# Kernel optimization log

Hardware: AMD Instinct MI355X
Metric: run time of the kernel (lower is better)

## Reference

```python
import jax, jax.numpy as jnp
import numpy as np


def setup_inputs() -> dict:
    key = jax.random.key(0)
    ks = jax.random.split(key, 6)
    B, F, E, H, U = 64, 4096, 256, 512, 512
    scale = 0.02
    return {
        "features": jax.random.normal(ks[0], (B, F, E), dtype=jnp.float32),
        "hidden": jax.random.normal(ks[1], (B, H), dtype=jnp.float32),
        "W1_w": jax.random.normal(ks[2], (E, U), dtype=jnp.float32) * scale,
        "W1_b": jnp.zeros((U,), dtype=jnp.float32),
        "W2_w": jax.random.normal(ks[3], (H, U), dtype=jnp.float32) * scale,
        "W2_b": jnp.zeros((U,), dtype=jnp.float32),
        "V_w": jax.random.normal(ks[4], (U, 1), dtype=jnp.float32) * scale,
        "V_b": jnp.zeros((1,), dtype=jnp.float32),
    }


def reference(features, hidden, W1_w, W1_b, W2_w, W2_b, V_w, V_b):
    # features: (B, F, E); hidden: (B, H)
    proj_f = jnp.einsum("bfe,eu->bfu", features, W1_w) + W1_b          # (B, F, U)
    proj_h = (hidden @ W2_w + W2_b)[:, None, :]                        # (B, 1, U)
    attention_hidden = jnp.tanh(proj_f + proj_h)                       # (B, F, U)
    scores = jnp.einsum("bfu,uo->bfo", attention_hidden, V_w) + V_b    # (B, F, 1)
    attention_weights = jax.nn.softmax(scores, axis=1)                 # (B, F, 1)
    context_vector = jnp.sum(attention_weights * features, axis=1)     # (B, E)
    return (context_vector, attention_weights)
```

## Files before the change

kernel.cpp:

```cpp
#include <hip/hip_runtime.h>
#include <cmath>

constexpr int Bdim = 64;
constexpr int Fdim = 4096;
constexpr int Edim = 256;
constexpr int Hdim = 512;
constexpr int Udim = 512;

typedef __attribute__((ext_vector_type(8))) short short8;
typedef __attribute__((ext_vector_type(4))) float f32x4;

__device__ __forceinline__ unsigned short f2bf(float f) {
    unsigned int u = __float_as_uint(f);
    u += 0x7FFFu + ((u >> 16) & 1u);
    return (unsigned short)(u >> 16);
}
__device__ __forceinline__ unsigned int pack2(float lo, float hi) {
    return (unsigned int)f2bf(lo) | ((unsigned int)f2bf(hi) << 16);
}
__device__ __forceinline__ float tanh_fast(float x) {
    float e = __expf(2.0f * x);
    return 1.0f - 2.0f * __builtin_amdgcn_rcpf(e + 1.0f);
}
__device__ __forceinline__ void gload_lds16(const void* g, void* l) {
    __builtin_amdgcn_global_load_lds(
        (const __attribute__((address_space(1))) unsigned int*)g,
        (__attribute__((address_space(3))) unsigned int*)l, 16, 0, 0);
}

__global__ __launch_bounds__(256) void prep_kernel(
    const float* __restrict__ hidden, const float* __restrict__ W2,
    const float* __restrict__ W1b, const float* __restrict__ W2b,
    float* __restrict__ cb,
    const float* __restrict__ W1, unsigned short* __restrict__ Th,
    float* __restrict__ ctx, const int do_t)
{
    const int bid = blockIdx.x;
    const int tid = threadIdx.x;

    if (bid < 128) {
        const int b = bid >> 1;
        const int u = (bid & 1) * 256 + tid;
        const float* hb = hidden + (size_t)b * Hdim;
        float acc = 0.f;
        #pragma unroll 8
        for (int h = 0; h < Hdim; ++h)
            acc = fmaf(hb[h], W2[(size_t)h * Udim + u], acc);
        cb[(size_t)b * Udim + u] = acc + W1b[u] + W2b[u];
    } else if (bid < 160) {
        if (!do_t) return;
        __shared__ unsigned short sT[64][72];
        const int k  = bid - 128;
        const int e0 = (k & 3) * 64, u0 = (k >> 2) * 64;
        const int ue = tid & 63, er = tid >> 6;
        #pragma unroll
        for (int it = 0; it < 16; ++it) {
            const int e = er + it * 4;
            sT[ue][e] = f2bf(W1[(size_t)(e0 + e) * Udim + u0 + ue]);
        }
        __syncthreads();
        const int ur = tid >> 2, cq = tid & 3;
        const int u = u0 + ur, s = u & 7;
        const int cA = (e0 >> 3) + cq * 2;
        uint4 a  = *(const uint4*)&sT[ur][cq * 16];
        uint4 b2 = *(const uint4*)&sT[ur][cq * 16 + 8];
        unsigned short* dst = Th + (size_t)u * Edim;
        *(uint4*)(dst + ((cA ^ s) << 3))       = a;
        *(uint4*)(dst + (((cA + 1) ^ s) << 3)) = b2;
    } else {
        const int idx = (bid - 160) * 256 + tid;
        ((float4*)ctx)[idx] = make_float4(0.f, 0.f, 0.f, 0.f);
    }
}

__global__ __launch_bounds__(256, 4) void score_mfma4_kernel(
    const float* __restrict__ feat,
    const unsigned short* __restrict__ W1Ts,
    const float* __restrict__ Vw, const float* __restrict__ Vb,
    const float* __restrict__ cb, float* __restrict__ scr,
    float* __restrict__ pm, float* __restrict__ ps, float* __restrict__ pc)
{
    __shared__ unsigned short lds[16896];

    const int b    = blockIdx.y;
    const int fc   = blockIdx.x;
    const int f0   = fc * 64;
    const int tid  = threadIdx.x;
    const int lane = tid & 63;
    const int w    = tid >> 6;
    const int ln15 = lane & 15;
    const int kq   = lane >> 4;
    const int swz  = ln15 & 7;

    short8 af[8];
    {
        unsigned short* sAw = lds + w * 4224;
        const float* gA = feat + ((size_t)(b * Fdim + f0 + w * 16)) * Edim;
        #pragma unroll
        for (int r = 0; r < 16; ++r) {
            float4 v = *(const float4*)(gA + (size_t)r * Edim + lane * 4);
            uint2 p; p.x = pack2(v.x, v.y); p.y = pack2(v.z, v.w);
            *(uint2*)&sAw[r * 264 + lane * 4] = p;
        }
        #pragma unroll
        for (int k8 = 0; k8 < 8; ++k8)
            af[k8] = *(const short8*)&sAw[ln15 * 264 + k8 * 32 + kq * 8];
    }
    __syncthreads();

    float sacc[4] = {};
    const float* cbB = cb + (size_t)b * Udim;

    {
        const char* gB = (const char*)W1Ts;
        #pragma unroll
        for (int t = 0; t < 4; ++t) {
            const int chunk = w * 4 + t;
            gload_lds16(gB + (size_t)chunk * 1024 + lane * 16,
                        (char*)lds + chunk * 1024);
        }
    }
    __syncthreads();

    for (int p = 0; p < 16; ++p) {
        if (p < 15) {
            const char* gB = (const char*)(W1Ts + (size_t)(p + 1) * 32 * Edim);
            char* lb = (char*)lds + ((p + 1) & 1) * 16384;
            #pragma unroll
            for (int t = 0; t < 4; ++t) {
                const int chunk = w * 4 + t;
                gload_lds16(gB + (size_t)chunk * 1024 + lane * 16,
                            lb + chunk * 1024);
            }
        }

        const unsigned short* bw = lds + (p & 1) * 8192;
        const int ub = p * 32;
        const float cu0 = cbB[ub + ln15],     cu1 = cbB[ub + 16 + ln15];
        const float vv0 = Vw[ub + ln15],      vv1 = Vw[ub + 16 + ln15];
        f32x4 acc0 = {}, acc1 = {};
        #pragma unroll
        for (int k8 = 0; k8 < 8; ++k8) {
            const int co = ((k8 * 4 + kq) ^ swz) * 8;
            short8 b0 = *(const short8*)&bw[ln15 * 256 + co];
            short8 b1 = *(const short8*)&bw[(16 + ln15) * 256 + co];
            acc0 = __builtin_amdgcn_mfma_f32_16x16x32_bf16(af[k8], b0, acc0, 0, 0, 0);
            acc1 = __builtin_amdgcn_mfma_f32_16x16x32_bf16(af[k8], b1, acc1, 0, 0, 0);
        }
        #pragma unroll
        for (int r = 0; r < 4; ++r)
            sacc[r] += tanh_fast(acc0[r] + cu0) * vv0
                     + tanh_fast(acc1[r] + cu1) * vv1;

        if (p < 15) __syncthreads();
    }

    float* sF = (float*)lds;
    float* wl = (float*)lds + 64;
    float4* sred = (float4*)((char*)lds + 1024);

    const float vb = Vb[0];
    #pragma unroll
    for (int r = 0; r < 4; ++r) {
        float s = sacc[r];
        s += __shfl_xor(s, 1);
        s += __shfl_xor(s, 2);
        s += __shfl_xor(s, 4);
        s += __shfl_xor(s, 8);
        if (ln15 == 0) {
            const int fr = w * 16 + kq * 4 + r;
            const float sv = s + vb;
            scr[(size_t)b * Fdim + f0 + fr] = sv;
            sF[fr] = sv;
        }
    }
    __syncthreads();

    if (tid < 64) {
        const float sc = sF[tid];
        float m = sc;
        #pragma unroll
        for (int off = 1; off < 64; off <<= 1)
            m = fmaxf(m, __shfl_xor(m, off));
        const float wv = expf(sc - m);
        float sm = wv;
        #pragma unroll
        for (int off = 1; off < 64; off <<= 1)
            sm += __shfl_xor(sm, off);
        wl[tid] = wv;
        if (tid == 0) {
            pm[b * 64 + fc] = m;
            ps[b * 64 + fc] = sm;
        }
    }
    __syncthreads();

    const int e4 = tid & 63;
    const int fg = tid >> 6;
    const float4* fp = (const float4*)(feat + ((size_t)b * Fdim + f0) * Edim);

    float4 a = make_float4(0.f, 0.f, 0.f, 0.f);
    #pragma unroll
    for (int i = 0; i < 16; ++i) {
        const int f = i * 4 + fg;
        const float4 fv = fp[(size_t)f * 64 + e4];
        const float wv = wl[f];
        a.x = fmaf(wv, fv.x, a.x);
        a.y = fmaf(wv, fv.y, a.y);
        a.z = fmaf(wv, fv.z, a.z);
        a.w = fmaf(wv, fv.w, a.w);
    }
    sred[tid] = a;
    __syncthreads();

    if (fg == 0) {
        const float4 r0 = sred[e4];
        const float4 r1 = sred[64 + e4];
        const float4 r2 = sred[128 + e4];
        const float4 r3 = sred[192 + e4];
        float4 o;
        o.x = r0.x + r1.x + r2.x + r3.x;
        o.y = r0.y + r1.y + r2.y + r3.y;
        o.z = r0.z + r1.z + r2.z + r3.z;
        o.w = r0.w + r1.w + r2.w + r3.w;
        *(float4*)&pc[((size_t)b * 64 + fc) * 256 + e4 * 4] = o;
    }
}

__global__ __launch_bounds__(256) void merge_kernel(
    const float* __restrict__ scr, const float* __restrict__ pm,
    const float* __restrict__ ps, const float* __restrict__ pc,
    float* __restrict__ wts, float* __restrict__ ctx)
{
    __shared__ float sscale[64];
    __shared__ float sms[2];

    const int b   = blockIdx.x;
    const int tid = threadIdx.x;

    if (tid < 64) {
        const float mi = pm[b * 64 + tid];
        float m = mi;
        #pragma unroll
        for (int off = 1; off < 64; off <<= 1)
            m = fmaxf(m, __shfl_xor(m, off));
        const float sc = expf(mi - m);
        float s = ps[b * 64 + tid] * sc;
        #pragma unroll
        for (int off = 1; off < 64; off <<= 1)
            s += __shfl_xor(s, off);
        sscale[tid] = sc;
        if (tid == 0) { sms[0] = m; sms[1] = 1.0f / s; }
    }
    __syncthreads();
    const float m   = sms[0];
    const float inv = sms[1];

    {
        float c = 0.f;
        const float* p = pc + (size_t)b * 64 * 256 + tid;
        #pragma unroll 8
        for (int i = 0; i < 64; ++i)
            c = fmaf(p[(size_t)i * 256], sscale[i], c);
        ctx[(size_t)b * Edim + tid] = c * inv;
    }

    const float* row  = scr + (size_t)b * Fdim;
    float*       wrow = wts + (size_t)b * Fdim;
    #pragma unroll
    for (int i = 0; i < 16; ++i) {
        const float v = row[tid + 256 * i];
        wrow[tid + 256 * i] = expf(v - m) * inv;
    }
}

constexpr int TFt = 64;
constexpr int TUt = 64;
constexpr int LDR = Edim + 4;

__global__ __launch_bounds__(256) void score_kernel(
    const float* __restrict__ feat, const float* __restrict__ W1,
    const float* __restrict__ Vw, const float* __restrict__ Vb,
    const float* __restrict__ cb, float* __restrict__ scores)
{
    __shared__ float sA[TFt * LDR];
    __shared__ float sW[TUt * LDR];

    const int b   = blockIdx.y;
    const int f0  = blockIdx.x * TFt;
    const int tid = threadIdx.x;
    const int tf  = tid >> 4;
    const int tu  = tid & 15;

    {
        const float4* gA = (const float4*)(feat + ((size_t)b * Fdim + f0) * Edim);
        #pragma unroll
        for (int it = 0; it < 16; ++it) {
            const int i = tid + it * 256;
            const int f = i >> 6;
            const int qq = i & 63;
            const float4 v = gA[i];
            *(float4*)&sA[f * LDR + 4 * qq] = v;
        }
    }

    float sacc[4] = {0.f, 0.f, 0.f, 0.f};
    const float* cbb = cb + (size_t)b * Udim;

    for (int uc = 0; uc < Udim; uc += TUt) {
        __syncthreads();
        #pragma unroll
        for (int it = 0; it < 16; ++it) {
            const int i = tid + it * 256;
            const int e = i >> 4;
            const int qq = i & 15;
            const float4 v = *(const float4*)(W1 + (size_t)e * Udim + uc + 4 * qq);
            sW[(4 * qq + 0) * LDR + e] = v.x;
            sW[(4 * qq + 1) * LDR + e] = v.y;
            sW[(4 * qq + 2) * LDR + e] = v.z;
            sW[(4 * qq + 3) * LDR + e] = v.w;
        }
        __syncthreads();

        float acc[4][4] = {};
        #pragma unroll 4
        for (int e = 0; e < Edim; e += 4) {
            float4 a0 = *(const float4*)&sA[(tf +  0) * LDR + e];
            float4 a1 = *(const float4*)&sA[(tf + 16) * LDR + e];
            float4 a2 = *(const float4*)&sA[(tf + 32) * LDR + e];
            float4 a3 = *(const float4*)&sA[(tf + 48) * LDR + e];
            float4 w0 = *(const float4*)&sW[(tu +  0) * LDR + e];
            float4 w1 = *(const float4*)&sW[(tu + 16) * LDR + e];
            float4 w2 = *(const float4*)&sW[(tu + 32) * LDR + e];
            float4 w3 = *(const float4*)&sW[(tu + 48) * LDR + e];
            #define FMA4(i, j, A, W)                         \
                acc[i][j] = fmaf(A.x, W.x, acc[i][j]);       \
                acc[i][j] = fmaf(A.y, W.y, acc[i][j]);       \
                acc[i][j] = fmaf(A.z, W.z, acc[i][j]);       \
                acc[i][j] = fmaf(A.w, W.w, acc[i][j]);
            FMA4(0,0,a0,w0) FMA4(0,1,a0,w1) FMA4(0,2,a0,w2) FMA4(0,3,a0,w3)
            FMA4(1,0,a1,w0) FMA4(1,1,a1,w1) FMA4(1,2,a1,w2) FMA4(1,3,a1,w3)
            FMA4(2,0,a2,w0) FMA4(2,1,a2,w1) FMA4(2,2,a2,w2) FMA4(2,3,a2,w3)
            FMA4(3,0,a3,w0) FMA4(3,1,a3,w1) FMA4(3,2,a3,w2) FMA4(3,3,a3,w3)
            #undef FMA4
        }

        #pragma unroll
        for (int j = 0; j < 4; ++j) {
            const int u = uc + tu + 16 * j;
            const float vw = Vw[u];
            const float cuv = cbb[u];
            #pragma unroll
            for (int i = 0; i < 4; ++i)
                sacc[i] = fmaf(tanhf(acc[i][j] + cuv), vw, sacc[i]);
        }
    }

    const float vb = Vb[0];
    #pragma unroll
    for (int i = 0; i < 4; ++i) {
        float s = sacc[i];
        s += __shfl_xor(s, 1);
        s += __shfl_xor(s, 2);
        s += __shfl_xor(s, 4);
        s += __shfl_xor(s, 8);
        if (tu == 0)
            scores[(size_t)b * Fdim + f0 + tf + 16 * i] = s + vb;
    }
}

__global__ __launch_bounds__(256) void softmax_kernel(float* __restrict__ sc)
{
    __shared__ float red[256];
    const int b = blockIdx.x;
    const int tid = threadIdx.x;
    float* row = sc + (size_t)b * Fdim;

    float v[16];
    float m = -INFINITY;
    #pragma unroll
    for (int i = 0; i < 16; ++i) {
        v[i] = row[tid + 256 * i];
        m = fmaxf(m, v[i]);
    }
    red[tid] = m;
    __syncthreads();
    for (int s = 128; s > 0; s >>= 1) {
        if (tid < s) red[tid] = fmaxf(red[tid], red[tid + s]);
        __syncthreads();
    }
    m = red[0];
    __syncthreads();

    float sum = 0.f;
    #pragma unroll
    for (int i = 0; i < 16; ++i) {
        v[i] = expf(v[i] - m);
        sum += v[i];
    }
    red[tid] = sum;
    __syncthreads();
    for (int s = 128; s > 0; s >>= 1) {
        if (tid < s) red[tid] += red[tid + s];
        __syncthreads();
    }
    const float inv = 1.f / red[0];
    #pragma unroll
    for (int i = 0; i < 16; ++i)
        row[tid + 256 * i] = v[i] * inv;
}

__global__ __launch_bounds__(256) void context_kernel(
    const float* __restrict__ feat, const float* __restrict__ wts,
    float* __restrict__ ctx)
{
    const int b  = blockIdx.y;
    const int fc = blockIdx.x;
    const int e  = threadIdx.x;

    const float* fp = feat + ((size_t)b * Fdim + (size_t)fc * 256) * Edim + e;
    const float* wp = wts + (size_t)b * Fdim + (size_t)fc * 256;

    float acc = 0.f;
    #pragma unroll 8
    for (int f = 0; f < 256; ++f)
        acc = fmaf(wp[f], fp[(size_t)f * Edim], acc);

    atomicAdd(&ctx[(size_t)b * Edim + e], acc);
}

extern "C" void kernel_launch(void* const* d_in, const int* in_sizes, int n_in,
                              void* d_out, int out_size, void* d_ws, size_t ws_size,
                              hipStream_t stream)
{
    const float* features = (const float*)d_in[0];
    const float* hidden   = (const float*)d_in[1];
    const float* W1w      = (const float*)d_in[2];
    const float* W1b      = (const float*)d_in[3];
    const float* W2w      = (const float*)d_in[4];
    const float* W2b      = (const float*)d_in[5];
    const float* Vw       = (const float*)d_in[6];
    const float* Vb       = (const float*)d_in[7];

    float* ctx = (float*)d_out;
    float* wts = (float*)d_out + (size_t)Bdim * Edim;

    float*          cb   = (float*)d_ws;
    unsigned short* W1Ts = (unsigned short*)((char*)d_ws + 131072);
    float*          scr  = (float*)((char*)d_ws + 393216);
    float*          pm   = (float*)((char*)d_ws + 1441792);
    float*          ps   = (float*)((char*)d_ws + 1458176);
    float*          pc   = (float*)((char*)d_ws + 1474560);
    const size_t NEED = 1474560 + (size_t)Bdim * 64 * Edim * sizeof(float);
    const int mfma_ok = (ws_size >= NEED) ? 1 : 0;

    prep_kernel<<<176, 256, 0, stream>>>(hidden, W2w, W1b, W2b, cb,
                                         W1w, W1Ts, ctx, mfma_ok);

    if (mfma_ok) {
        dim3 sgrid(Fdim / 64, Bdim);
        score_mfma4_kernel<<<sgrid, 256, 0, stream>>>(features, W1Ts, Vw, Vb, cb,
                                                      scr, pm, ps, pc);
        merge_kernel<<<Bdim, 256, 0, stream>>>(scr, pm, ps, pc, wts, ctx);
    } else {
        dim3 sgrid(Fdim / TFt, Bdim);
        score_kernel<<<sgrid, 256, 0, stream>>>(features, W1w, Vw, Vb, cb, wts);
        softmax_kernel<<<Bdim, 256, 0, stream>>>(wts);
        dim3 cgrid(16, Bdim);
        context_kernel<<<cgrid, 256, 0, stream>>>(features, wts, ctx);
    }
}
```

Measured before the change: 464.6 us.

## Use 2-wave blocks with 32 rows per wave sharing each W1 fragment

```diff
diff --git a/kernel.cpp b/kernel.cpp
--- a/kernel.cpp
+++ b/kernel.cpp
@@ -1,4 +1,5 @@
 #include <hip/hip_runtime.h>
+#include <hip/hip_bf16.h>
 #include <cmath>
 
 constexpr int Bdim = 64;
@@ -16,7 +17,8 @@
     return (unsigned short)(u >> 16);
 }
 __device__ __forceinline__ unsigned int pack2(float lo, float hi) {
-    return (unsigned int)f2bf(lo) | ((unsigned int)f2bf(hi) << 16);
+    __hip_bfloat162 h2 = __float22bfloat162_rn(make_float2(lo, hi));
+    return *reinterpret_cast<unsigned int*>(&h2);
 }
 __device__ __forceinline__ float tanh_fast(float x) {
     float e = __expf(2.0f * x);
@@ -73,14 +75,14 @@
     }
 }
 
-__global__ __launch_bounds__(256, 4) void score_mfma4_kernel(
+__global__ __launch_bounds__(128, 4) void score_mfma4_kernel(
     const float* __restrict__ feat,
     const unsigned short* __restrict__ W1Ts,
     const float* __restrict__ Vw, const float* __restrict__ Vb,
     const float* __restrict__ cb, float* __restrict__ scr,
     float* __restrict__ pm, float* __restrict__ ps, float* __restrict__ pc)
 {
-    __shared__ unsigned short lds[16896];
+    __shared__ unsigned short lds[8192];
 
     const int b    = blockIdx.y;
     const int fc   = blockIdx.x;
@@ -92,97 +94,97 @@
     const int kq   = lane >> 4;
     const int swz  = ln15 & 7;
 
-    short8 af[8];
+    #pragma unroll
+    for (int t = 0; t < 4; ++t)
+        gload_lds16((const char*)W1Ts + (size_t)(tid + t * 128) * 16,
+                    (char*)lds + (tid + t * 128) * 16);
+
+    short8 af[2][8];
     {
-        unsigned short* sAw = lds + w * 4224;
-        const float* gA = feat + ((size_t)(b * Fdim + f0 + w * 16)) * Edim;
-        #pragma unroll
-        for (int r = 0; r < 16; ++r) {
-            float4 v = *(const float4*)(gA + (size_t)r * Edim + lane * 4);
-            uint2 p; p.x = pack2(v.x, v.y); p.y = pack2(v.z, v.w);
-            *(uint2*)&sAw[r * 264 + lane * 4] = p;
-        }
-        #pragma unroll
-        for (int k8 = 0; k8 < 8; ++k8)
-            af[k8] = *(const short8*)&sAw[ln15 * 264 + k8 * 32 + kq * 8];
-    }
-    __syncthreads();
-
-    float sacc[4] = {};
+        const float* gA = feat +
+            ((size_t)(b * Fdim + f0 + w * 32 + ln15)) * Edim + kq * 8;
+        #pragma unroll
+        for (int h = 0; h < 2; ++h) {
+            #pragma unroll 4
+            for (int k8 = 0; k8 < 8; ++k8) {
+                const float* p = gA + (size_t)h * 16 * Edim + k8 * 32;
+                const float4 v0 = *(const float4*)(p);
+                const float4 v1 = *(const float4*)(p + 4);
+                uint4 uu;
+                uu.x = pack2(v0.x, v0.y);
+                uu.y = pack2(v0.z, v0.w);
+                uu.z = pack2(v1.x, v1.y);
+                uu.w = pack2(v1.z, v1.w);
+                af[h][k8] = *reinterpret_cast<short8*>(&uu);
+            }
+        }
+    }
+    __syncthreads();
+
+    float sacc[2][4] = {};
     const float* cbB = cb + (size_t)b * Udim;
 
-    {
-        const char* gB = (const char*)W1Ts;
-        #pragma unroll
-        for (int t = 0; t < 4; ++t) {
-            const int chunk = w * 4 + t;
-            gload_lds16(gB + (size_t)chunk * 1024 + lane * 16,
-                        (char*)lds + chunk * 1024);
-        }
-    }
-    __syncthreads();
-
-    for (int p = 0; p < 16; ++p) {
-        if (p < 15) {
-            const char* gB = (const char*)(W1Ts + (size_t)(p + 1) * 32 * Edim);
-            char* lb = (char*)lds + ((p + 1) & 1) * 16384;
+    for (int p = 0; p < 32; ++p) {
+        if (p < 31) {
+            const char* gB = (const char*)(W1Ts + (size_t)(p + 1) * 16 * Edim);
+            char* lb = (char*)lds + ((p + 1) & 1) * 8192;
             #pragma unroll
-            for (int t = 0; t < 4; ++t) {
-                const int chunk = w * 4 + t;
-                gload_lds16(gB + (size_t)chunk * 1024 + lane * 16,
-                            lb + chunk * 1024);
-            }
-        }
-
-        const unsigned short* bw = lds + (p & 1) * 8192;
-        const int ub = p * 32;
-        const float cu0 = cbB[ub + ln15],     cu1 = cbB[ub + 16 + ln15];
-        const float vv0 = Vw[ub + ln15],      vv1 = Vw[ub + 16 + ln15];
+            for (int t = 0; t < 4; ++t)
+                gload_lds16(gB + (size_t)(tid + t * 128) * 16,
+                            lb + (tid + t * 128) * 16);
+        }
+
+        const unsigned short* bw = lds + (p & 1) * 4096;
+        const int ub = p * 16;
+        const float cu0 = cbB[ub + ln15];
+        const float vv0 = Vw[ub + ln15];
         f32x4 acc0 = {}, acc1 = {};
         #pragma unroll
         for (int k8 = 0; k8 < 8; ++k8) {
             const int co = ((k8 * 4 + kq) ^ swz) * 8;
             short8 b0 = *(const short8*)&bw[ln15 * 256 + co];
-            short8 b1 = *(const short8*)&bw[(16 + ln15) * 256 + co];
-            acc0 = __builtin_amdgcn_mfma_f32_16x16x32_bf16(af[k8], b0, acc0, 0, 0, 0);
-            acc1 = __builtin_amdgcn_mfma_f32_16x16x32_bf16(af[k8], b1, acc1, 0, 0, 0);
-        }
-        #pragma unroll
-        for (int r = 0; r < 4; ++r)
-            sacc[r] += tanh_fast(acc0[r] + cu0) * vv0
-                     + tanh_fast(acc1[r] + cu1) * vv1;
-
-        if (p < 15) __syncthreads();
+            acc0 = __builtin_amdgcn_mfma_f32_16x16x32_bf16(af[0][k8], b0, acc0, 0, 0, 0);
+            acc1 = __builtin_amdgcn_mfma_f32_16x16x32_bf16(af[1][k8], b0, acc1, 0, 0, 0);
+        }
+        #pragma unroll
+        for (int r = 0; r < 4; ++r) {
+            sacc[0][r] += tanh_fast(acc0[r] + cu0) * vv0;
+            sacc[1][r] += tanh_fast(acc1[r] + cu0) * vv0;
+        }
+
+        if (p < 31) __syncthreads();
     }
 
     float* sF = (float*)lds;
     float* wl = (float*)lds + 64;
-    float4* sred = (float4*)((char*)lds + 1024);
+    float4* sred = (float4*)((char*)lds + 512);
 
     const float vb = Vb[0];
     #pragma unroll
-    for (int r = 0; r < 4; ++r) {
-        float s = sacc[r];
-        s += __shfl_xor(s, 1);
-        s += __shfl_xor(s, 2);
-        s += __shfl_xor(s, 4);
-        s += __shfl_xor(s, 8);
-        if (ln15 == 0) {
-            const int fr = w * 16 + kq * 4 + r;
-            const float sv = s + vb;
-            scr[(size_t)b * Fdim + f0 + fr] = sv;
-            sF[fr] = sv;
-        }
-    }
+    for (int mi = 0; mi < 2; ++mi)
+        #pragma unroll
+        for (int r = 0; r < 4; ++r) {
+            float s = sacc[mi][r];
+            s += __shfl_xor(s, 1);
+            s += __shfl_xor(s, 2);
+            s += __shfl_xor(s, 4);
+            s += __shfl_xor(s, 8);
+            if (ln15 == 0) {
+                const int fr = w * 32 + mi * 16 + kq * 4 + r;
+                const float sv = s + vb;
+                scr[(size_t)b * Fdim + f0 + fr] = sv;
+                sF[fr] = sv;
+            }
+        }
     __syncthreads();
 
     if (tid < 64) {
-        const float sc = sF[tid];
-        float m = sc;
+        const float sc_ = sF[tid];
+        float m = sc_;
         #pragma unroll
         for (int off = 1; off < 64; off <<= 1)
             m = fmaxf(m, __shfl_xor(m, off));
-        const float wv = expf(sc - m);
+        const float wv = expf(sc_ - m);
         float sm = wv;
         #pragma unroll
         for (int off = 1; off < 64; off <<= 1)
@@ -195,15 +197,12 @@
     }
     __syncthreads();
 
-    const int e4 = tid & 63;
-    const int fg = tid >> 6;
     const float4* fp = (const float4*)(feat + ((size_t)b * Fdim + f0) * Edim);
-
     float4 a = make_float4(0.f, 0.f, 0.f, 0.f);
-    #pragma unroll
-    for (int i = 0; i < 16; ++i) {
-        const int f = i * 4 + fg;
-        const float4 fv = fp[(size_t)f * 64 + e4];
+    #pragma unroll 8
+    for (int i = 0; i < 32; ++i) {
+        const int f = w * 32 + i;
+        const float4 fv = fp[(size_t)f * 64 + lane];
         const float wv = wl[f];
         a.x = fmaf(wv, fv.x, a.x);
         a.y = fmaf(wv, fv.y, a.y);
@@ -213,17 +212,15 @@
     sred[tid] = a;
     __syncthreads();
 
-    if (fg == 0) {
-        const float4 r0 = sred[e4];
-        const float4 r1 = sred[64 + e4];
-        const float4 r2 = sred[128 + e4];
-        const float4 r3 = sred[192 + e4];
+    if (w == 0) {
+        const float4 r0 = sred[lane];
+        const float4 r1 = sred[64 + lane];
         float4 o;
-        o.x = r0.x + r1.x + r2.x + r3.x;
-        o.y = r0.y + r1.y + r2.y + r3.y;
-        o.z = r0.z + r1.z + r2.z + r3.z;
-        o.w = r0.w + r1.w + r2.w + r3.w;
-        *(float4*)&pc[((size_t)b * 64 + fc) * 256 + e4 * 4] = o;
+        o.x = r0.x + r1.x;
+        o.y = r0.y + r1.y;
+        o.z = r0.z + r1.z;
+        o.w = r0.w + r1.w;
+        *(float4*)&pc[((size_t)b * 64 + fc) * 256 + lane * 4] = o;
     }
 }
 
@@ -459,7 +456,7 @@
 
     if (mfma_ok) {
         dim3 sgrid(Fdim / 64, Bdim);
-        score_mfma4_kernel<<<sgrid, 256, 0, stream>>>(features, W1Ts, Vw, Vb, cb,
+        score_mfma4_kernel<<<sgrid, 128, 0, stream>>>(features, W1Ts, Vw, Vb, cb,
                                                       scr, pm, ps, pc);
         merge_kernel<<<Bdim, 256, 0, stream>>>(scr, pm, ps, pc, wts, ctx);
     } else {
```

Measured after the change: 926.1 us. 1.99x slower.
